# Optimization experiments

Hardware: AMD Instinct MI355X
Metric: run time of the kernel (lower is better)

The kernel has to match this reference:

```python
import jax, jax.numpy as jnp
import numpy as np

N_CLASSES = 4
ALPHA = 2.0
BIG = jnp.float32(1e9)  # stands in for +inf at non-site pixels


def _dt1d_sq(f):
    # Exact 1D squared distance transform along the last axis:
    # out[i] = min_j f[j] + (i - j)^2  (brute-force lower envelope, fully vectorized)
    n = f.shape[-1]
    i = jnp.arange(n, dtype=f.dtype)
    d2 = (i[:, None] - i[None, :]) ** 2  # [n, n]
    return jnp.min(f[..., None, :] + d2, axis=-1)


def _edt_sq(sites):
    # Exact squared Euclidean distance to the nearest True pixel (separable 2D DT).
    f = jnp.where(sites, jnp.float32(0.0), BIG)
    f = _dt1d_sq(f)                                  # pass along W
    f = jnp.swapaxes(_dt1d_sq(jnp.swapaxes(f, -1, -2)), -1, -2)  # pass along H
    return f


def _distance_field(img):
    # Mirrors HausdorffDTLoss.distance_field:
    #   fg_dist = edt(fg_mask)  (distance to nearest bg pixel, 0 on bg)
    #   bg_dist = edt(~fg_mask) (distance to nearest fg pixel, 0 on fg)
    #   field = fg_dist + bg_dist if fg_mask.any() else 0
    fg = img > 0.5                                   # [B, H, W] bool
    fg_dist = jnp.sqrt(_edt_sq(~fg))                 # dist to nearest background
    bg_dist = jnp.sqrt(_edt_sq(fg))                  # dist to nearest foreground
    any_fg = jnp.any(fg, axis=(-2, -1), keepdims=True)
    return jnp.where(any_fg, fg_dist + bg_dist, jnp.float32(0.0))


def reference(pred, target):
    # pred: [B, 4, H, W] logits; target: [B, H, W] int labels in [0, 4)
    probs = jax.nn.softmax(pred, axis=1)
    tgt = jnp.moveaxis(jax.nn.one_hot(target, N_CLASSES, dtype=probs.dtype), -1, 1)  # [B,4,H,W]
    total = jnp.float32(0.0)
    for i in range(N_CLASSES):
        p = probs[:, i]
        t = tgt[:, i]
        pred_dt = jax.lax.stop_gradient(_distance_field(p))
        target_dt = jax.lax.stop_gradient(_distance_field(t))
        pred_error = (p - t) ** 2
        distance = pred_dt ** ALPHA + target_dt ** ALPHA
        total = total + jnp.mean(pred_error * distance)
    return total / N_CLASSES


def setup_inputs() -> dict:
    key = jax.random.key(0)
    k1, k2 = jax.random.split(key)
    pred = jax.random.normal(k1, (4, 4, 256, 256), dtype=jnp.float32)
    target = jax.random.randint(k2, (4, 256, 256), 0, 4).astype(jnp.int32)
    return {"pred": pred, "target": target}
```

## Files before the change

kernel.cpp:

```cpp
#include <hip/hip_runtime.h>

#define HH 256
#define WW 256
#define NB 4
#define NC 4
#define NPIX (HH*WW)
#define NIMG (NB*NC)
#define TOTAL (NB*NC*HH*WW)
#define INF_G (1<<30)
#define PAD 257

__device__ __forceinline__ float wave_reduce(float v) {
    #pragma unroll
    for (int off = 32; off > 0; off >>= 1) v += __shfl_down(v, off);
    return v;
}

__device__ __forceinline__ int nearest_dist(const unsigned long long* m, int x) {
    int best = 0x7fffffff;
    #pragma unroll
    for (int w = 0; w < 4; ++w) {
        unsigned long long mm = m[w];
        if (!mm) continue;
        int rel = x - (w << 6);
        unsigned long long lmask = (rel >= 63) ? ~0ull
                                 : ((rel < 0) ? 0ull : ((2ull << (rel & 63)) - 1ull));
        unsigned long long lm = mm & lmask;
        if (lm) best = min(best, rel - (63 - __clzll(lm)));
        unsigned long long rmask = (rel <= 0) ? ~0ull
                                 : ((rel > 63) ? 0ull : (~0ull << (rel & 63)));
        unsigned long long rm = mm & rmask;
        if (rm) best = min(best, (__ffsll((long long)rm) - 1) - rel);
    }
    return best;
}

__global__ void build_masks(const float* __restrict__ pred, const int* __restrict__ target,
                            unsigned long long* __restrict__ masks, float* __restrict__ out) {
    int blk = blockIdx.x;
    int b = blk >> 8, y = blk & 255;
    int x = threadIdx.x;

    if (blk == 0 && x == 0) out[0] = 0.0f;

    const float* base = pred + (((size_t)b * NC) * HH + y) * WW + x;
    float v0 = base[0 * (size_t)NPIX];
    float v1 = base[1 * (size_t)NPIX];
    float v2 = base[2 * (size_t)NPIX];
    float v3 = base[3 * (size_t)NPIX];
    float m = fmaxf(fmaxf(v0, v1), fmaxf(v2, v3));
    float e0 = expf(v0 - m), e1 = expf(v1 - m), e2 = expf(v2 - m), e3 = expf(v3 - m);
    float inv = 1.0f / (e0 + e1 + e2 + e3);
    float p[4] = { e0 * inv, e1 * inv, e2 * inv, e3 * inv };

    int tc = target[((size_t)b * HH + y) * WW + x];

    __shared__ unsigned long long sm[NC][2][4];
    int lane = x & 63, wv = x >> 6;
    #pragma unroll
    for (int c = 0; c < 4; ++c) {
        unsigned long long bp = __ballot(p[c] > 0.5f);
        unsigned long long bt = __ballot(tc == c);
        if (lane == 0) { sm[c][0][wv] = bp; sm[c][1][wv] = bt; }
    }
    __syncthreads();

    if (x < 32) {
        int c = x >> 3, s = (x >> 2) & 1, w = x & 3;
        masks[((((size_t)(b * NC + c)) * 2 + s) * 4 + w) * HH + y] = sm[c][s][w];
    }
}

__global__ __launch_bounds__(512) void cols_loss(const unsigned long long* __restrict__ masks,
                                                 const float* __restrict__ pred,
                                                 float* __restrict__ out) {
    int bid = blockIdx.x;
    int img = bid >> 4;
    int xbase = (bid & 15) << 4;
    int b = img >> 2, c = img & 3;
    int t = threadIdx.x;
    int lane = t & 63, wv = t >> 6;

    __shared__ unsigned long long sm[2048];
    __shared__ int hP[16 * PAD], hT[16 * PAD];
    __shared__ float pe_s[16 * PAD];
    __shared__ int sF[2][8];
    __shared__ float sred[8];

    const unsigned long long* mb = masks + (size_t)img * 2048;
    #pragma unroll
    for (int j = 0; j < 4; ++j) sm[t + 512 * j] = mb[t + 512 * j];
    __syncthreads();

    bool anyP = false, anyT = false;
    if (t < 256) {
        unsigned long long rp = sm[0 * HH + t] | sm[1 * HH + t] | sm[2 * HH + t] | sm[3 * HH + t];
        unsigned long long rt = sm[4 * HH + t] | sm[5 * HH + t] | sm[6 * HH + t] | sm[7 * HH + t];
        anyP = (rp != 0ull); anyT = (rt != 0ull);
    }
    unsigned long long bP = __ballot(anyP), bT = __ballot(anyT);
    if (lane == 0) { sF[0][wv] = (bP != 0ull); sF[1][wv] = (bT != 0ull); }

    for (int j = 0; j < 8; ++j) {
        int idx = t + 512 * j;
        int cx = idx & 15, y = idx >> 4;
        int x = xbase + cx;

        unsigned long long mp[4], mt[4];
        #pragma unroll
        for (int w = 0; w < 4; ++w) {
            mp[w] = sm[w * HH + y];
            mt[w] = sm[(4 + w) * HH + y];
        }
        int fgP = (int)((mp[x >> 6] >> (x & 63)) & 1);
        int fgT = (int)((mt[x >> 6] >> (x & 63)) & 1);

        unsigned long long sel[4];
        unsigned long long flip = fgP ? ~0ull : 0ull;
        #pragma unroll
        for (int w = 0; w < 4; ++w) sel[w] = mp[w] ^ flip;
        int dP = nearest_dist(sel, x);
        int vP = (dP > 255) ? INF_G : dP * dP;
        hP[cx * PAD + y] = vP | (fgP << 31);

        flip = fgT ? ~0ull : 0ull;
        #pragma unroll
        for (int w = 0; w < 4; ++w) sel[w] = mt[w] ^ flip;
        int dT = nearest_dist(sel, x);
        int vT = (dT > 255) ? INF_G : dT * dT;
        hT[cx * PAD + y] = vT | (fgT << 31);

        const float* basep = pred + ((size_t)b * NC) * NPIX + (size_t)y * WW + x;
        float v0 = basep[0 * (size_t)NPIX];
        float v1 = basep[1 * (size_t)NPIX];
        float v2 = basep[2 * (size_t)NPIX];
        float v3 = basep[3 * (size_t)NPIX];
        float m = fmaxf(fmaxf(v0, v1), fmaxf(v2, v3));
        float e0 = expf(v0 - m), e1 = expf(v1 - m), e2 = expf(v2 - m), e3 = expf(v3 - m);
        float inv = 1.0f / (e0 + e1 + e2 + e3);
        float pc = (c == 0) ? e0 * inv : (c == 1) ? e1 * inv : (c == 2) ? e2 * inv : e3 * inv;
        float d = pc - (float)fgT;
        pe_s[cx * PAD + y] = d * d;
    }
    __syncthreads();

    int hs1 = sF[0][0] | sF[0][1] | sF[0][2] | sF[0][3] | sF[0][4] | sF[0][5] | sF[0][6] | sF[0][7];
    int hs3 = sF[1][0] | sF[1][1] | sF[1][2] | sF[1][3] | sF[1][4] | sF[1][5] | sF[1][6] | sF[1][7];

    float acc = 0.0f;
    int y = t & 255, cg = t >> 8;
    for (int i = 0; i < 8; ++i) {
        int cx = cg * 8 + i;
        const int* hp = &hP[cx * PAD];
        const int* ht = &hT[cx * PAD];

        int selfP = hp[y];
        int msP = selfP & 0x80000000;
        int best = selfP & 0x7fffffff;
        for (int s = 1; s < HH; ++s) {
            int ss = s * s;
            if (ss >= best) break;
            int jm = y - s, jp = y + s;
            if (jm >= 0) {
                int hsv = hp[jm];
                int cand = (((hsv ^ msP) & 0x80000000) == 0) ? (hsv & 0x7fffffff) + ss : ss;
                best = min(best, cand);
            }
            if (jp < HH) {
                int hsv = hp[jp];
                int cand = (((hsv ^ msP) & 0x80000000) == 0) ? (hsv & 0x7fffffff) + ss : ss;
                best = min(best, cand);
            }
        }
        float dtP = (best >= INF_G) ? sqrtf(1.0e9f) : sqrtf((float)best);

        int selfT = ht[y];
        int msT = selfT & 0x80000000;
        best = selfT & 0x7fffffff;
        for (int s = 1; s < HH; ++s) {
            int ss = s * s;
            if (ss >= best) break;
            int jm = y - s, jp = y + s;
            if (jm >= 0) {
                int hsv = ht[jm];
                int cand = (((hsv ^ msT) & 0x80000000) == 0) ? (hsv & 0x7fffffff) + ss : ss;
                best = min(best, cand);
            }
            if (jp < HH) {
                int hsv = ht[jp];
                int cand = (((hsv ^ msT) & 0x80000000) == 0) ? (hsv & 0x7fffffff) + ss : ss;
                best = min(best, cand);
            }
        }
        float dtT = (best >= INF_G) ? sqrtf(1.0e9f) : sqrtf((float)best);

        float pd = hs1 ? dtP : 0.0f;
        float td = hs3 ? dtT : 0.0f;
        acc += pe_s[cx * PAD + y] * (pd * pd + td * td);
    }

    acc = wave_reduce(acc);
    if (lane == 0) sred[wv] = acc;
    __syncthreads();
    if (t == 0) {
        float bs = sred[0] + sred[1] + sred[2] + sred[3] + sred[4] + sred[5] + sred[6] + sred[7];
        unsafeAtomicAdd(out, bs * (1.0f / (float)TOTAL));
    }
}

extern "C" void kernel_launch(void* const* d_in, const int* in_sizes, int n_in,
                              void* d_out, int out_size, void* d_ws, size_t ws_size,
                              hipStream_t stream) {
    const float* pred  = (const float*)d_in[0];
    const int* target  = (const int*)d_in[1];
    float* out = (float*)d_out;

    unsigned long long* masks = (unsigned long long*)d_ws;

    build_masks<<<NB * HH, 256, 0, stream>>>(pred, target, masks, out);
    cols_loss<<<NIMG * 16, 512, 0, stream>>>(masks, pred, out);
}
```

Baseline: 34.82 us.

## Fuse mask build and column loss into one cooperative kernel with grid sync

Merges the two kernels into a single cooperative launch of 256 blocks. Each block first builds the row bitmasks for four image rows, then all blocks wait on a grid-wide barrier before running the column distance-transform and loss phase. This removes one kernel launch and the gap between the two kernels. In exchange it adds a grid.sync, the overhead of a cooperative launch, and writes the masks with direct global stores instead of staging them through shared memory.

```diff
diff --git a/kernel.cpp b/kernel.cpp
--- a/kernel.cpp
+++ b/kernel.cpp
@@ -1,4 +1,7 @@
 #include <hip/hip_runtime.h>
+#include <hip/hip_cooperative_groups.h>
+
+namespace cg = cooperative_groups;
 
 #define HH 256
 #define WW 256
@@ -35,57 +38,61 @@
     return best;
 }
 
-__global__ void build_masks(const float* __restrict__ pred, const int* __restrict__ target,
-                            unsigned long long* __restrict__ masks, float* __restrict__ out) {
-    int blk = blockIdx.x;
-    int b = blk >> 8, y = blk & 255;
-    int x = threadIdx.x;
-
-    if (blk == 0 && x == 0) out[0] = 0.0f;
-
-    const float* base = pred + (((size_t)b * NC) * HH + y) * WW + x;
-    float v0 = base[0 * (size_t)NPIX];
-    float v1 = base[1 * (size_t)NPIX];
-    float v2 = base[2 * (size_t)NPIX];
-    float v3 = base[3 * (size_t)NPIX];
-    float m = fmaxf(fmaxf(v0, v1), fmaxf(v2, v3));
-    float e0 = expf(v0 - m), e1 = expf(v1 - m), e2 = expf(v2 - m), e3 = expf(v3 - m);
-    float inv = 1.0f / (e0 + e1 + e2 + e3);
-    float p[4] = { e0 * inv, e1 * inv, e2 * inv, e3 * inv };
-
-    int tc = target[((size_t)b * HH + y) * WW + x];
-
-    __shared__ unsigned long long sm[NC][2][4];
-    int lane = x & 63, wv = x >> 6;
-    #pragma unroll
-    for (int c = 0; c < 4; ++c) {
-        unsigned long long bp = __ballot(p[c] > 0.5f);
-        unsigned long long bt = __ballot(tc == c);
-        if (lane == 0) { sm[c][0][wv] = bp; sm[c][1][wv] = bt; }
-    }
-    __syncthreads();
-
-    if (x < 32) {
-        int c = x >> 3, s = (x >> 2) & 1, w = x & 3;
-        masks[((((size_t)(b * NC + c)) * 2 + s) * 4 + w) * HH + y] = sm[c][s][w];
-    }
-}
-
-__global__ __launch_bounds__(512) void cols_loss(const unsigned long long* __restrict__ masks,
-                                                 const float* __restrict__ pred,
-                                                 float* __restrict__ out) {
+__global__ __launch_bounds__(512) void fused_all(
+        const float* __restrict__ pred, const int* __restrict__ target,
+        unsigned long long* __restrict__ masks, float* __restrict__ out) {
+    cg::grid_group grid = cg::this_grid();
     int bid = blockIdx.x;
-    int img = bid >> 4;
-    int xbase = (bid & 15) << 4;
-    int b = img >> 2, c = img & 3;
     int t = threadIdx.x;
     int lane = t & 63, wv = t >> 6;
+
+    if (bid == 0 && t == 0) out[0] = 0.0f;
+
+    {
+        int x = t & 255;
+        int half = t >> 8;
+        int w = x >> 6;
+        #pragma unroll
+        for (int j = 0; j < 2; ++j) {
+            int ru = bid * 4 + half * 2 + j;
+            int b = ru >> 8, y = ru & 255;
+
+            const float* base = pred + (((size_t)b * NC) * HH + y) * WW + x;
+            float v0 = base[0 * (size_t)NPIX];
+            float v1 = base[1 * (size_t)NPIX];
+            float v2 = base[2 * (size_t)NPIX];
+            float v3 = base[3 * (size_t)NPIX];
+            float m = fmaxf(fmaxf(v0, v1), fmaxf(v2, v3));
+            float e0 = expf(v0 - m), e1 = expf(v1 - m), e2 = expf(v2 - m), e3 = expf(v3 - m);
+            float inv = 1.0f / (e0 + e1 + e2 + e3);
+            float p[4] = { e0 * inv, e1 * inv, e2 * inv, e3 * inv };
+
+            int tc = target[((size_t)b * HH + y) * WW + x];
+
+            #pragma unroll
+            for (int c = 0; c < 4; ++c) {
+                unsigned long long bp = __ballot(p[c] > 0.5f);
+                unsigned long long bt = __ballot(tc == c);
+                if ((x & 63) == 0) {
+                    size_t mi = ((size_t)(b * NC + c)) * 2;
+                    masks[((mi + 0) * 4 + w) * HH + y] = bp;
+                    masks[((mi + 1) * 4 + w) * HH + y] = bt;
+                }
+            }
+        }
+    }
+
+    grid.sync();
 
     __shared__ unsigned long long sm[2048];
     __shared__ int hP[16 * PAD], hT[16 * PAD];
     __shared__ float pe_s[16 * PAD];
     __shared__ int sF[2][8];
     __shared__ float sred[8];
+
+    int img = bid >> 4;
+    int xbase = (bid & 15) << 4;
+    int b = img >> 2, c = img & 3;
 
     const unsigned long long* mb = masks + (size_t)img * 2048;
     #pragma unroll
@@ -148,9 +155,9 @@
     int hs3 = sF[1][0] | sF[1][1] | sF[1][2] | sF[1][3] | sF[1][4] | sF[1][5] | sF[1][6] | sF[1][7];
 
     float acc = 0.0f;
-    int y = t & 255, cg = t >> 8;
+    int y = t & 255, cg2 = t >> 8;
     for (int i = 0; i < 8; ++i) {
-        int cx = cg * 8 + i;
+        int cx = cg2 * 8 + i;
         const int* hp = &hP[cx * PAD];
         const int* ht = &hT[cx * PAD];
 
@@ -217,6 +224,7 @@
 
     unsigned long long* masks = (unsigned long long*)d_ws;
 
-    build_masks<<<NB * HH, 256, 0, stream>>>(pred, target, masks, out);
-    cols_loss<<<NIMG * 16, 512, 0, stream>>>(masks, pred, out);
-}
+    void* args[] = { (void*)&pred, (void*)&target, (void*)&masks, (void*)&out };
+    hipLaunchCooperativeKernel((const void*)fused_all, dim3(256), dim3(512),
+                               args, 0, stream);
+}
```

Measured after the change: 63.20 us. +81.5%, slower.
